# Optimization experiments

Hardware: AMD Instinct MI355X
Metric: run time of the kernel (lower is better)

## Reference

```python
import jax, jax.numpy as jnp
import numpy as np

B, L, D, H = 2, 2048, 1024, 16
HD = D // H  # head dim = 64


def setup_inputs() -> dict:
    key = jax.random.key(0)
    ks = jax.random.split(key, 6)
    s = 0.02
    return {
        "hidden_states": jax.random.normal(ks[0], (B, L, D), jnp.float32),
        "attention_mask": jnp.zeros((B, 1, 1, L), jnp.float32),
        "Wq": jax.random.normal(ks[1], (D, D), jnp.float32) * s,
        "bq": jnp.zeros((D,), jnp.float32),
        "Wk": jax.random.normal(ks[2], (D, D), jnp.float32) * s,
        "bk": jnp.zeros((D,), jnp.float32),
        "Wv": jax.random.normal(ks[3], (D, D), jnp.float32) * s,
        "bv": jnp.zeros((D,), jnp.float32),
        "Wo": jax.random.normal(ks[4], (D, D), jnp.float32) * s,
        "bo": jnp.zeros((D,), jnp.float32),
    }


def reference(hidden_states, attention_mask, Wq, bq, Wk, bk, Wv, bv, Wo, bo):
    # Linear projections (torch Linear: x @ W.T + b; here W stored as [in,out])
    q = hidden_states @ Wq + bq  # [B,L,D]
    k = hidden_states @ Wk + bk
    v = hidden_states @ Wv + bv

    def split_heads(x):  # [B,L,D] -> [B,H,L,HD]
        return x.reshape(B, L, H, HD).transpose(0, 2, 1, 3)

    q, k, v = split_heads(q), split_heads(k), split_heads(v)

    scores = jnp.einsum("bhqd,bhkd->bhqk", q, k) / jnp.sqrt(
        jnp.asarray(HD, q.dtype)
    )
    scores = scores + attention_mask  # additive mask, broadcast [B,1,1,L]
    pdtype = scores.dtype
    # fp32 upcast around softmax, as in the original module
    probs = jax.nn.softmax(scores.astype(jnp.float32), axis=-1).astype(pdtype)
    # dropout prob = 0 (eval) -> identity; head_mask=None
    ctx = jnp.einsum("bhqk,bhkd->bhqd", probs, v)  # [B,H,L,HD]
    ctx = ctx.transpose(0, 2, 1, 3).reshape(B, L, D)
    out = ctx @ Wo + bo  # BertSelfOutput_preLN dense (dropout=0)
    return out
```

## Files before the change

kernel.cpp:

```cpp
#include <hip/hip_runtime.h>

#define BB 2
#define LL 2048
#define DDIM 1024
#define HH 16
#define HDIM 64
#define MM (BB*LL)
#define KK 1024
#define LOG2E 1.44269504f

typedef __attribute__((ext_vector_type(8))) short s8v;
typedef __attribute__((ext_vector_type(8))) unsigned short u8v;
typedef __attribute__((ext_vector_type(4))) float f4v;
typedef __attribute__((ext_vector_type(16))) float f16v;

__device__ __forceinline__ unsigned short f2bf(float f) {
    unsigned int u = __float_as_uint(f);
    u += 0x7fffu + ((u >> 16) & 1u);
    return (unsigned short)(u >> 16);
}

__device__ __forceinline__ float fexp2(float x) { return __builtin_amdgcn_exp2f(x); }

__device__ __forceinline__ void gld_lds16(const unsigned short* g, unsigned short* l) {
    __builtin_amdgcn_global_load_lds(
        (const __attribute__((address_space(1))) unsigned int*)g,
        (__attribute__((address_space(3))) unsigned int*)l, 16, 0, 0);
}

__global__ __launch_bounds__(256) void prep(
        const float* __restrict__ X,
        const float* __restrict__ Wq, const float* __restrict__ Wk,
        const float* __restrict__ Wv, const float* __restrict__ Wo,
        unsigned short* __restrict__ Xb,
        unsigned short* __restrict__ WqT, unsigned short* __restrict__ WkT,
        unsigned short* __restrict__ WvT, unsigned short* __restrict__ WoT) {
    __shared__ float lds[64][65];
    const int blk = blockIdx.x, t = threadIdx.x;
    if (blk < 4096) {
        int i = blk * 256 + t;
        float4 v = ((const float4*)X)[i];
        ushort4 r;
        r.x = f2bf(v.x); r.y = f2bf(v.y); r.z = f2bf(v.z); r.w = f2bf(v.w);
        ((ushort4*)Xb)[i] = r;
        return;
    }
    const int tb = blk - 4096;
    const int w = tb >> 8;
    const int tile = tb & 255;
    const int k0 = (tile >> 4) * 64, n0 = (tile & 15) * 64;
    const float* src; unsigned short* dst;
    switch (w) {
        case 0: src = Wq; dst = WqT; break;
        case 1: src = Wk; dst = WkT; break;
        case 2: src = Wv; dst = WvT; break;
        default: src = Wo; dst = WoT; break;
    }
    #pragma unroll
    for (int j = 0; j < 4; ++j) {
        int r = (t >> 4) + 16*j, c = (t & 15) * 4;
        float4 v = *(const float4*)(src + (size_t)(k0 + r) * DDIM + n0 + c);
        lds[r][c] = v.x; lds[r][c+1] = v.y; lds[r][c+2] = v.z; lds[r][c+3] = v.w;
    }
    __syncthreads();
    #pragma unroll
    for (int j = 0; j < 2; ++j) {
        int rr = (t >> 3) + 32*j, cc = (t & 7) * 8;
        u8v o;
        #pragma unroll
        for (int i = 0; i < 8; ++i) o[i] = f2bf(lds[cc + i][rr]);
        *(u8v*)(dst + (size_t)(n0 + rr) * KK + k0 + cc) = o;
    }
}

__device__ __forceinline__ void gemm_core(const unsigned short* __restrict__ A,
                                          const unsigned short* __restrict__ BT,
                                          int Mbase, int Nbase,
                                          unsigned short* As, unsigned short* Bs,
                                          f4v acc[4][4]) {
    const int t = threadIdx.x;
    const int lane = t & 63, wave = t >> 6;
    const int wm = wave & 1, wn = wave >> 1;
    const int l15 = lane & 15, quad = lane >> 4;
    const int srow = t >> 2, schunk = (t & 3) * 8;

    #pragma unroll
    for (int mt = 0; mt < 4; ++mt)
        #pragma unroll
        for (int nt = 0; nt < 4; ++nt)
            acc[mt][nt] = f4v{0.f, 0.f, 0.f, 0.f};

    const unsigned short* gA0 = A  + (size_t)(Mbase + srow)      * KK + schunk;
    const unsigned short* gA1 = A  + (size_t)(Mbase + 64 + srow) * KK + schunk;
    const unsigned short* gB0 = BT + (size_t)(Nbase + srow)      * KK + schunk;
    const unsigned short* gB1 = BT + (size_t)(Nbase + 64 + srow) * KK + schunk;
    unsigned short* lA0 = As + t*8;
    unsigned short* lA1 = As + 64*32 + t*8;
    unsigned short* lB0 = Bs + t*8;
    unsigned short* lB1 = Bs + 64*32 + t*8;

    for (int kb = 0; kb < KK; kb += 32) {
        __syncthreads();
        gld_lds16(gA0 + kb, lA0);
        gld_lds16(gA1 + kb, lA1);
        gld_lds16(gB0 + kb, lB0);
        gld_lds16(gB1 + kb, lB1);
        __syncthreads();
        s8v af[4], bfv[4];
        #pragma unroll
        for (int mt = 0; mt < 4; ++mt)
            af[mt] = *(const s8v*)(As + (wm*64 + mt*16 + l15)*32 + quad*8);
        #pragma unroll
        for (int nt = 0; nt < 4; ++nt)
            bfv[nt] = *(const s8v*)(Bs + (wn*64 + nt*16 + l15)*32 + quad*8);
        #pragma unroll
        for (int mt = 0; mt < 4; ++mt)
            #pragma unroll
            for (int nt = 0; nt < 4; ++nt)
                acc[mt][nt] = __builtin_amdgcn_mfma_f32_16x16x32_bf16(af[mt], bfv[nt], acc[mt][nt], 0, 0, 0);
    }
}

__global__ __launch_bounds__(256) void qkv_gemm(
        const unsigned short* __restrict__ Xb,
        const unsigned short* __restrict__ WqT, const unsigned short* __restrict__ WkT,
        const unsigned short* __restrict__ WvT,
        const float* __restrict__ bq, const float* __restrict__ bk, const float* __restrict__ bv,
        unsigned short* __restrict__ Qh, unsigned short* __restrict__ Kh,
        unsigned short* __restrict__ Vt) {
    __shared__ alignas(16) unsigned short smem[64*136 > 128*64 ? 64*136 : 128*64];
    unsigned short* As = smem;
    unsigned short* Bs = smem + 128*32;
    const int mode = blockIdx.z;
    const unsigned short* BT = (mode == 0) ? WqT : (mode == 1) ? WkT : WvT;
    const float* bias        = (mode == 0) ? bq  : (mode == 1) ? bk  : bv;
    unsigned short* out      = (mode == 0) ? Qh  : (mode == 1) ? Kh  : Vt;
    const int Mbase = blockIdx.y * 128, Nbase = blockIdx.x * 128;

    f4v acc[4][4];
    gemm_core(Xb, BT, Mbase, Nbase, As, Bs, acc);

    const int t = threadIdx.x;
    const int lane = t & 63, wave = t >> 6;
    const int wm = wave & 1, wn = wave >> 1, l15 = lane & 15, quad = lane >> 4;

    float bl[4];
    #pragma unroll
    for (int nt = 0; nt < 4; ++nt) bl[nt] = bias[Nbase + wn*64 + nt*16 + l15];

    #pragma unroll
    for (int h2 = 0; h2 < 2; ++h2) {
        __syncthreads();
        if (wm == h2) {
            #pragma unroll
            for (int mt = 0; mt < 4; ++mt)
                #pragma unroll
                for (int nt = 0; nt < 4; ++nt)
                    #pragma unroll
                    for (int r = 0; r < 4; ++r) {
                        int trow = mt*16 + quad*4 + r;
                        int fcol = wn*64 + nt*16 + l15;
                        smem[trow*136 + fcol] = f2bf(acc[mt][nt][r] + bl[nt]);
                    }
        }
        __syncthreads();
        const int gmbase = Mbase + h2*64;
        if (mode == 2) {
            int f = t >> 1, tc = (t & 1) * 32;
            int gn = Nbase + f;
            int hh = gn >> 6, dd = gn & 63;
            int gm0 = gmbase + tc;
            int bb = gm0 >> 11, ll0 = gm0 & 2047;
            unsigned short* dst = out + ((size_t)(bb*HH + hh)*HDIM + dd)*LL + ll0;
            #pragma unroll
            for (int c = 0; c < 4; ++c) {
                u8v o8;
                #pragma unroll
                for (int i = 0; i < 8; ++i)
                    o8[i] = smem[(tc + c*8 + i)*136 + f];
                *(u8v*)(dst + c*8) = o8;
            }
        } else {
            int tt = t >> 2, fc = (t & 3) * 32;
            int gm = gmbase + tt;
            int bb = gm >> 11, ll = gm & 2047;
            #pragma unroll
            for (int c = 0; c < 4; ++c) {
                int gn = Nbase + fc + c*8;
                int hh = gn >> 6, dd = gn & 63;
                u8v o8 = *(u8v*)(smem + tt*136 + fc + c*8);
                *(u8v*)(out + ((size_t)(bb*HH + hh)*LL + ll)*HDIM + dd) = o8;
            }
        }
    }
}

__global__ __launch_bounds__(256) void attn(
        const unsigned short* __restrict__ Qh, const unsigned short* __restrict__ Kh,
        const unsigned short* __restrict__ Vt, const float* __restrict__ mask,
        unsigned short* __restrict__ ctx) {
    __shared__ alignas(16) unsigned short Ks[64*72];
    __shared__ alignas(16) unsigned short Vs[64*72];
    __shared__ alignas(16) unsigned short P [4*32*72];

    const int t = threadIdx.x, lane = t & 63, wave = t >> 6;
    const int l31 = lane & 31, hgrp = lane >> 5;

    const int n = blockIdx.x;
    const int bh = (n & 7) * 4 + ((n >> 3) & 3);
    const int qblk = n >> 5;
    const int b = bh >> 4, hh = bh & 15;

    const unsigned short* Qb = Qh + (size_t)bh * LL * HDIM;
    const unsigned short* Kb = Kh + (size_t)bh * LL * HDIM;
    const unsigned short* Vb = Vt + (size_t)bh * HDIM * LL;
    const float* mb = mask + (size_t)b * LL;
    const int q0 = qblk * 128 + wave * 32;
    unsigned short* Pw = P + wave * 32 * 72;

    const int srow = t >> 2, scol = (t & 3) * 16;

    s8v qf[4];
    #pragma unroll
    for (int hf = 0; hf < 4; ++hf)
        qf[hf] = *(const s8v*)(Qb + (size_t)(q0 + l31)*HDIM + hf*16 + hgrp*8);

    f16v o[2];
    #pragma unroll
    for (int nc = 0; nc < 2; ++nc)
        #pragma unroll
        for (int r = 0; r < 16; ++r) o[nc][r] = 0.f;
    float rs[16];
    #pragma unroll
    for (int r = 0; r < 16; ++r) rs[r] = 0.f;

    const float C1 = 0.125f * LOG2E;

    for (int kt = 0; kt < LL; kt += 64) {
        float4 ka  = *(const float4*)(Kb + (size_t)(kt + srow)*HDIM + scol);
        float4 kb2 = *(const float4*)(Kb + (size_t)(kt + srow)*HDIM + scol + 8);
        float4 va  = *(const float4*)(Vb + (size_t)srow*LL + kt + scol);
        float4 vb2 = *(const float4*)(Vb + (size_t)srow*LL + kt + scol + 8);
        float mv0 = mb[kt + l31] * LOG2E;
        float mv1 = mb[kt + 32 + l31] * LOG2E;

        __syncthreads();
        *(float4*)(Ks + srow*72 + scol)     = ka;
        *(float4*)(Ks + srow*72 + scol + 8) = kb2;
        *(float4*)(Vs + srow*72 + scol)     = va;
        *(float4*)(Vs + srow*72 + scol + 8) = vb2;
        __syncthreads();

        f16v sac[2];
        #pragma unroll
        for (int kc = 0; kc < 2; ++kc) {
            #pragma unroll
            for (int r = 0; r < 16; ++r) sac[kc][r] = 0.f;
            #pragma unroll
            for (int hf = 0; hf < 4; ++hf) {
                s8v kf = *(const s8v*)(Ks + (kc*32 + l31)*72 + hf*16 + hgrp*8);
                sac[kc] = __builtin_amdgcn_mfma_f32_32x32x16_bf16(qf[hf], kf, sac[kc], 0, 0, 0);
            }
        }
        #pragma unroll
        for (int kc = 0; kc < 2; ++kc) {
            float mvv = kc ? mv1 : mv0;
            #pragma unroll
            for (int r = 0; r < 16; ++r) {
                float p = fexp2(sac[kc][r] * C1 + mvv);
                rs[r] += p;
                int row = (r & 3) + 8*(r >> 2) + 4*hgrp;
                Pw[row*72 + kc*32 + l31] = (unsigned short)(__float_as_uint(p) >> 16);
            }
        }
        #pragma unroll
        for (int kt16 = 0; kt16 < 4; ++kt16) {
            s8v pf = *(const s8v*)(Pw + l31*72 + kt16*16 + hgrp*8);
            #pragma unroll
            for (int nc = 0; nc < 2; ++nc) {
                s8v vf = *(const s8v*)(Vs + (nc*32 + l31)*72 + kt16*16 + hgrp*8);
                o[nc] = __builtin_amdgcn_mfma_f32_32x32x16_bf16(pf, vf, o[nc], 0, 0, 0);
            }
        }
    }

    #pragma unroll
    for (int r = 0; r < 16; ++r) {
        float s0 = rs[r];
        s0 += __shfl_xor(s0, 1);
        s0 += __shfl_xor(s0, 2);
        s0 += __shfl_xor(s0, 4);
        s0 += __shfl_xor(s0, 8);
        s0 += __shfl_xor(s0, 16);
        rs[r] = 1.0f / s0;
    }
    #pragma unroll
    for (int r = 0; r < 16; ++r) {
        int row = (r & 3) + 8*(r >> 2) + 4*hgrp;
        int q = q0 + row;
        size_t base = ((size_t)b*LL + q)*DDIM + hh*HDIM;
        #pragma unroll
        for (int nc = 0; nc < 2; ++nc)
            ctx[base + nc*32 + l31] = f2bf(o[nc][r] * rs[r]);
    }
}

__global__ __launch_bounds__(256) void out_gemm(
        const unsigned short* __restrict__ Cb, const unsigned short* __restrict__ WoT,
        const float* __restrict__ bo, float* __restrict__ out) {
    __shared__ alignas(16) unsigned short As[128*32];
    __shared__ alignas(16) unsigned short Bs[64*32];
    const int t = threadIdx.x;
    const int lane = t & 63, wave = t >> 6;
    const int wm = wave & 1, wn = wave >> 1;
    const int l15 = lane & 15, quad = lane >> 4;
    const int srow = t >> 2, schunk = (t & 3) * 8;
    const int Mbase = blockIdx.y * 128, Nbase = blockIdx.x * 64;

    f4v acc[4][2];
    #pragma unroll
    for (int mt = 0; mt < 4; ++mt)
        #pragma unroll
        for (int nt = 0; nt < 2; ++nt)
            acc[mt][nt] = f4v{0.f, 0.f, 0.f, 0.f};

    const unsigned short* gA0 = Cb  + (size_t)(Mbase + srow)      * KK + schunk;
    const unsigned short* gA1 = Cb  + (size_t)(Mbase + 64 + srow) * KK + schunk;
    const unsigned short* gB0 = WoT + (size_t)(Nbase + srow)      * KK + schunk;
    unsigned short* lA0 = As + t*8;
    unsigned short* lA1 = As + 64*32 + t*8;
    unsigned short* lB0 = Bs + t*8;

    for (int kb = 0; kb < KK; kb += 32) {
        __syncthreads();
        gld_lds16(gA0 + kb, lA0);
        gld_lds16(gA1 + kb, lA1);
        gld_lds16(gB0 + kb, lB0);
        __syncthreads();
        s8v af[4], bfv[2];
        #pragma unroll
        for (int mt = 0; mt < 4; ++mt)
            af[mt] = *(const s8v*)(As + (wm*64 + mt*16 + l15)*32 + quad*8);
        #pragma unroll
        for (int nt = 0; nt < 2; ++nt)
            bfv[nt] = *(const s8v*)(Bs + (wn*32 + nt*16 + l15)*32 + quad*8);
        #pragma unroll
        for (int mt = 0; mt < 4; ++mt)
            #pragma unroll
            for (int nt = 0; nt < 2; ++nt)
                acc[mt][nt] = __builtin_amdgcn_mfma_f32_16x16x32_bf16(af[mt], bfv[nt], acc[mt][nt], 0, 0, 0);
    }

    #pragma unroll
    for (int mt = 0; mt < 4; ++mt)
        #pragma unroll
        for (int nt = 0; nt < 2; ++nt)
            #pragma unroll
            for (int r = 0; r < 4; ++r) {
                int gm = Mbase + wm*64 + mt*16 + quad*4 + r;
                int gn = Nbase + wn*32 + nt*16 + l15;
                out[(size_t)gm*DDIM + gn] = acc[mt][nt][r] + bo[gn];
            }
}

extern "C" void kernel_launch(void* const* d_in, const int* in_sizes, int n_in,
                              void* d_out, int out_size, void* d_ws, size_t ws_size,
                              hipStream_t stream) {
    const float* X    = (const float*)d_in[0];
    const float* mask = (const float*)d_in[1];
    const float* Wq   = (const float*)d_in[2];
    const float* bq   = (const float*)d_in[3];
    const float* Wk   = (const float*)d_in[4];
    const float* bk   = (const float*)d_in[5];
    const float* Wv   = (const float*)d_in[6];
    const float* bv   = (const float*)d_in[7];
    const float* Wo   = (const float*)d_in[8];
    const float* bo   = (const float*)d_in[9];
    float* out = (float*)d_out;

    char* ws = (char*)d_ws;
    unsigned short* Xb  = (unsigned short*)(ws);
    unsigned short* WqT = (unsigned short*)(ws + (8u  << 20));
    unsigned short* WkT = (unsigned short*)(ws + (10u << 20));
    unsigned short* WvT = (unsigned short*)(ws + (12u << 20));
    unsigned short* WoT = (unsigned short*)(ws + (14u << 20));
    unsigned short* Qh  = (unsigned short*)(ws + (16u << 20));
    unsigned short* Kh  = (unsigned short*)(ws + (24u << 20));
    unsigned short* Vt  = (unsigned short*)(ws + (32u << 20));
    unsigned short* Cb  = Xb;

    prep     <<<dim3(5120),    dim3(256), 0, stream>>>(X, Wq, Wk, Wv, Wo, Xb, WqT, WkT, WvT, WoT);
    qkv_gemm <<<dim3(8,32,3),  dim3(256), 0, stream>>>(Xb, WqT, WkT, WvT, bq, bk, bv, Qh, Kh, Vt);
    attn     <<<dim3(512),     dim3(256), 0, stream>>>(Qh, Kh, Vt, mask, Cb);
    out_gemm <<<dim3(16,32),   dim3(256), 0, stream>>>(Cb, WoT, bo, out);
}
```

Before: 222.9 us.

## Remap GEMM blocks across XCDs for L2 locality and drop LDS-staged epilogue

Both projection GEMMs now use a flat 1-D grid and remap block indices so that blocks landing on the same XCD (assigned round-robin by index mod 8) share A row panels and weight column tiles, to improve per-XCD L2 reuse. The QKV epilogue no longer stages results through shared memory with two barrier rounds for coalesced 16-byte stores. It writes scalar bf16 values straight from registers, which removes the barriers and LDS traffic but produces scattered 2-byte stores. For the transposed V layout those stores are strided by the sequence length.

```diff
diff --git a/kernel.cpp b/kernel.cpp
--- a/kernel.cpp
+++ b/kernel.cpp
@@ -128,71 +128,43 @@
         const float* __restrict__ bq, const float* __restrict__ bk, const float* __restrict__ bv,
         unsigned short* __restrict__ Qh, unsigned short* __restrict__ Kh,
         unsigned short* __restrict__ Vt) {
-    __shared__ alignas(16) unsigned short smem[64*136 > 128*64 ? 64*136 : 128*64];
-    unsigned short* As = smem;
-    unsigned short* Bs = smem + 128*32;
-    const int mode = blockIdx.z;
+    __shared__ alignas(16) unsigned short As[128*32];
+    __shared__ alignas(16) unsigned short Bs[128*32];
+
+    const int n = blockIdx.x;
+    const int xcd = n & 7, r = n >> 3;
+    const int gx = xcd >> 1, gy = xcd & 1;
+    const int mode = r % 3;
+    const int r2 = r / 3;
+    const int x = gx*2 + (r2 & 1);
+    const int y = gy*16 + (r2 >> 1);
+
     const unsigned short* BT = (mode == 0) ? WqT : (mode == 1) ? WkT : WvT;
     const float* bias        = (mode == 0) ? bq  : (mode == 1) ? bk  : bv;
     unsigned short* out      = (mode == 0) ? Qh  : (mode == 1) ? Kh  : Vt;
-    const int Mbase = blockIdx.y * 128, Nbase = blockIdx.x * 128;
+    const int Mbase = y * 128, Nbase = x * 128;
 
     f4v acc[4][4];
     gemm_core(Xb, BT, Mbase, Nbase, As, Bs, acc);
 
-    const int t = threadIdx.x;
-    const int lane = t & 63, wave = t >> 6;
+    const int lane = threadIdx.x & 63, wave = threadIdx.x >> 6;
     const int wm = wave & 1, wn = wave >> 1, l15 = lane & 15, quad = lane >> 4;
-
-    float bl[4];
-    #pragma unroll
-    for (int nt = 0; nt < 4; ++nt) bl[nt] = bias[Nbase + wn*64 + nt*16 + l15];
-
-    #pragma unroll
-    for (int h2 = 0; h2 < 2; ++h2) {
-        __syncthreads();
-        if (wm == h2) {
-            #pragma unroll
-            for (int mt = 0; mt < 4; ++mt)
-                #pragma unroll
-                for (int nt = 0; nt < 4; ++nt)
-                    #pragma unroll
-                    for (int r = 0; r < 4; ++r) {
-                        int trow = mt*16 + quad*4 + r;
-                        int fcol = wn*64 + nt*16 + l15;
-                        smem[trow*136 + fcol] = f2bf(acc[mt][nt][r] + bl[nt]);
-                    }
-        }
-        __syncthreads();
-        const int gmbase = Mbase + h2*64;
-        if (mode == 2) {
-            int f = t >> 1, tc = (t & 1) * 32;
-            int gn = Nbase + f;
-            int hh = gn >> 6, dd = gn & 63;
-            int gm0 = gmbase + tc;
-            int bb = gm0 >> 11, ll0 = gm0 & 2047;
-            unsigned short* dst = out + ((size_t)(bb*HH + hh)*HDIM + dd)*LL + ll0;
-            #pragma unroll
-            for (int c = 0; c < 4; ++c) {
-                u8v o8;
-                #pragma unroll
-                for (int i = 0; i < 8; ++i)
-                    o8[i] = smem[(tc + c*8 + i)*136 + f];
-                *(u8v*)(dst + c*8) = o8;
-            }
-        } else {
-            int tt = t >> 2, fc = (t & 3) * 32;
-            int gm = gmbase + tt;
-            int bb = gm >> 11, ll = gm & 2047;
-            #pragma unroll
-            for (int c = 0; c < 4; ++c) {
-                int gn = Nbase + fc + c*8;
-                int hh = gn >> 6, dd = gn & 63;
-                u8v o8 = *(u8v*)(smem + tt*136 + fc + c*8);
-                *(u8v*)(out + ((size_t)(bb*HH + hh)*LL + ll)*HDIM + dd) = o8;
-            }
-        }
-    }
+    #pragma unroll
+    for (int mt = 0; mt < 4; ++mt)
+        #pragma unroll
+        for (int nt = 0; nt < 4; ++nt)
+            #pragma unroll
+            for (int rr = 0; rr < 4; ++rr) {
+                int gm = Mbase + wm*64 + mt*16 + quad*4 + rr;
+                int gn = Nbase + wn*64 + nt*16 + l15;
+                float v = acc[mt][nt][rr] + bias[gn];
+                int bb = gm >> 11, ll = gm & 2047;
+                int hh = gn >> 6,  dd = gn & 63;
+                if (mode == 2)
+                    out[((size_t)(bb*HH + hh)*HDIM + dd)*LL + ll] = f2bf(v);
+                else
+                    out[((size_t)(bb*HH + hh)*LL + ll)*HDIM + dd] = f2bf(v);
+            }
 }
 
 __global__ __launch_bounds__(256) void attn(
@@ -315,7 +287,12 @@
     const int wm = wave & 1, wn = wave >> 1;
     const int l15 = lane & 15, quad = lane >> 4;
     const int srow = t >> 2, schunk = (t & 3) * 8;
-    const int Mbase = blockIdx.y * 128, Nbase = blockIdx.x * 64;
+
+    const int n = blockIdx.x;
+    const int xcd = n & 7, r0 = n >> 3;
+    const int x = r0 & 15, ysub = r0 >> 4;
+    const int y = ysub * 8 + xcd;
+    const int Mbase = y * 128, Nbase = x * 64;
 
     f4v acc[4][2];
     #pragma unroll
@@ -356,10 +333,10 @@
         #pragma unroll
         for (int nt = 0; nt < 2; ++nt)
             #pragma unroll
-            for (int r = 0; r < 4; ++r) {
-                int gm = Mbase + wm*64 + mt*16 + quad*4 + r;
+            for (int rr = 0; rr < 4; ++rr) {
+                int gm = Mbase + wm*64 + mt*16 + quad*4 + rr;
                 int gn = Nbase + wn*32 + nt*16 + l15;
-                out[(size_t)gm*DDIM + gn] = acc[mt][nt][r] + bo[gn];
+                out[(size_t)gm*DDIM + gn] = acc[mt][nt][rr] + bo[gn];
             }
 }
 
@@ -389,8 +366,8 @@
     unsigned short* Vt  = (unsigned short*)(ws + (32u << 20));
     unsigned short* Cb  = Xb;
 
-    prep     <<<dim3(5120),    dim3(256), 0, stream>>>(X, Wq, Wk, Wv, Wo, Xb, WqT, WkT, WvT, WoT);
-    qkv_gemm <<<dim3(8,32,3),  dim3(256), 0, stream>>>(Xb, WqT, WkT, WvT, bq, bk, bv, Qh, Kh, Vt);
-    attn     <<<dim3(512),     dim3(256), 0, stream>>>(Qh, Kh, Vt, mask, Cb);
-    out_gemm <<<dim3(16,32),   dim3(256), 0, stream>>>(Cb, WoT, bo, out);
-}
+    prep     <<<dim3(5120),  dim3(256), 0, stream>>>(X, Wq, Wk, Wv, Wo, Xb, WqT, WkT, WvT, WoT);
+    qkv_gemm <<<dim3(768),   dim3(256), 0, stream>>>(Xb, WqT, WkT, WvT, bq, bk, bv, Qh, Kh, Vt);
+    attn     <<<dim3(512),   dim3(256), 0, stream>>>(Qh, Kh, Vt, mask, Cb);
+    out_gemm <<<dim3(512),   dim3(256), 0, stream>>>(Cb, WoT, bo, out);
+}
```

Result: faster. 209.8 us (-5.9%).
